# Optimization experiments

Hardware: AMD Instinct MI355X
Metric: run time of the kernel (lower is better)

Reference implementation:

```python
import jax, jax.numpy as jnp
import numpy as np

PAD_IDX = 0
NUM_VISITS, MAX_CODES = 16384, 48
VOCAB, DIM, HID = 20000, 128, 128


def setup_inputs() -> dict:
    key = jax.random.key(0)
    ks = jax.random.split(key, 16)
    ids = jax.random.randint(ks[0], (NUM_VISITS, MAX_CODES), 0, VOCAB)
    # guarantee every visit has at least one non-pad code (original returns
    # zeros for empty visits; we simply avoid that degenerate case)
    ids = ids.at[:, 0].set(jnp.maximum(ids[:, 0], 1))
    s = 0.05
    return {
        "ids": ids,
        "emb": jax.random.normal(ks[1], (VOCAB, DIM), jnp.float32) * s,
        "W1": jax.random.normal(ks[2], (DIM, HID), jnp.float32) * s,
        "b1": jnp.zeros((HID,), jnp.float32),
        "W2": jax.random.normal(ks[3], (HID, HID), jnp.float32) * s,
        "b2": jnp.zeros((HID,), jnp.float32),
        "Wa1": jax.random.normal(ks[4], (HID, HID), jnp.float32) * s,
        "ba1": jnp.zeros((HID,), jnp.float32),
        "wa2": jax.random.normal(ks[5], (HID,), jnp.float32) * s,
        "ba2": jnp.zeros((1,), jnp.float32),
        "Wr1": jax.random.normal(ks[6], (HID, HID), jnp.float32) * s,
        "br1": jnp.zeros((HID,), jnp.float32),
        "Wr2": jax.random.normal(ks[7], (HID, DIM), jnp.float32) * s,
        "br2": jnp.zeros((DIM,), jnp.float32),
    }


def reference(ids, emb, W1, b1, W2, b2, Wa1, ba1, wa2, ba2, Wr1, br1, Wr2, br2):
    # ids: [V, C] padded code indices; pad_idx codes are masked out.
    mask = ids != PAD_IDX                              # [V, C]
    x = emb[ids]                                       # [V, C, D]
    # phi: Linear->SiLU->Linear->SiLU
    h = jax.nn.silu(x @ W1 + b1)
    h = jax.nn.silu(h @ W2 + b2)                       # [V, C, H]
    # attention pooling: Linear->Tanh->Linear(1), masked softmax over codes
    a = jnp.tanh(h @ Wa1 + ba1) @ wa2 + ba2[0]         # [V, C]
    a = jnp.where(mask, a, -jnp.inf)
    a = jax.nn.softmax(a, axis=1)                      # pad rows -> weight 0
    h_pool = jnp.einsum("vc,vch->vh", a, h)            # [V, H]
    # rho: Linear->SiLU->Linear
    v = jax.nn.silu(h_pool @ Wr1 + br1) @ Wr2 + br2    # [V, D]
    return v
```

## Files before the change

kernel.cpp:

```cpp
#include <hip/hip_runtime.h>
#include <math.h>


#define DIM 128
#define MT 16
#define XLDP 136

typedef float f32x4 __attribute__((ext_vector_type(4)));
typedef short short8 __attribute__((ext_vector_type(8)));
typedef unsigned short u16x8 __attribute__((ext_vector_type(8)));

#define MFMA(a, b, c) __builtin_amdgcn_mfma_f32_16x16x32_bf16(a, b, c, 0, 0, 0)

__device__ __forceinline__ float fast_rcp(float x) {
  return __builtin_amdgcn_rcpf(x);
}
__device__ __forceinline__ float silu_f(float v) {
  return v * fast_rcp(1.0f + __expf(-v));
}
__device__ __forceinline__ float tanh_f(float v) {
  float t = __expf(2.0f * v);
  return 1.0f - 2.0f * fast_rcp(t + 1.0f);
}

__device__ __forceinline__ unsigned short bf16_hi(float x, float* hif) {
  unsigned u = __builtin_bit_cast(unsigned, x);
  unsigned h = (u + 0x8000u) >> 16;
  *hif = __builtin_bit_cast(float, h << 16);
  return (unsigned short)h;
}
__device__ __forceinline__ unsigned short bf16_rd(float x) {
  unsigned u = __builtin_bit_cast(unsigned, x);
  return (unsigned short)((u + 0x8000u) >> 16);
}
__device__ __forceinline__ unsigned short f2h(float x) {
  return __builtin_bit_cast(unsigned short, (_Float16)x);
}
__device__ __forceinline__ float h2f(unsigned short u) {
  return (float)__builtin_bit_cast(_Float16, u);
}

__global__ __launch_bounds__(256) void prep_wfrags(
    const float* __restrict__ W1, const float* __restrict__ W2,
    const float* __restrict__ Wa1, const float* __restrict__ Wr1,
    const float* __restrict__ Wr2, unsigned short* __restrict__ frags) {
  const int m = blockIdx.x >> 3, chunk = blockIdx.x & 7;
  const float* W = (m == 0) ? W1 : (m == 1) ? W2 : (m == 2) ? Wa1
                  : (m == 3) ? Wr1 : Wr2;
  unsigned short* fh = frags + (size_t)m * 32768;
  unsigned short* fl = fh + 16384;
  const int fid = chunk * 256 + threadIdx.x;
  const int lane = fid & 63, s = (fid >> 6) & 3, t = fid >> 8;
  const int k0 = s * 32 + (lane >> 4) * 8;
  const int n = t * 16 + (lane & 15);
#pragma unroll
  for (int j = 0; j < 8; ++j) {
    float w = W[(size_t)(k0 + j) * DIM + n];
    float hf;
    unsigned short h = bf16_hi(w, &hf);
    fh[fid * 8 + j] = h;
    fl[fid * 8 + j] = bf16_rd(w - hf);
  }
}

__device__ __forceinline__ void stage_bf16(const float* __restrict__ src,
                                           unsigned short (*xh)[XLDP],
                                           unsigned short (*xl)[XLDP],
                                           int tid) {
  const float4* s = (const float4*)src;
#pragma unroll
  for (int tph = 0; tph < 2; ++tph) {
    int idx = tid + tph * 256;
    int r = idx >> 5, c4 = idx & 31;
    float4 v = s[idx];
    float hf;
    ushort4 h, l;
    h.x = bf16_hi(v.x, &hf); l.x = bf16_rd(v.x - hf);
    h.y = bf16_hi(v.y, &hf); l.y = bf16_rd(v.y - hf);
    h.z = bf16_hi(v.z, &hf); l.z = bf16_rd(v.z - hf);
    h.w = bf16_hi(v.w, &hf); l.w = bf16_rd(v.w - hf);
    *(ushort4*)&xh[r][c4 * 4] = h;
    *(ushort4*)&xl[r][c4 * 4] = l;
  }
}

template <int NT>
__device__ __forceinline__ void gemm_frag(const unsigned short (*xh)[XLDP],
                                          const unsigned short (*xl)[XLDP],
                                          const unsigned short* __restrict__ bhp,
                                          const unsigned short* __restrict__ blp,
                                          int tt0, int lane, f32x4 acc[NT]) {
  const int cr = lane & 15, g = lane >> 4;
  short8 ah[4], al[4];
#pragma unroll
  for (int s = 0; s < 4; ++s) {
    ah[s] = *(const short8*)&xh[cr][s * 32 + g * 8];
    al[s] = *(const short8*)&xl[cr][s * 32 + g * 8];
  }
#pragma unroll
  for (int t = 0; t < NT; ++t) {
    short8 bh[4], bl[4];
#pragma unroll
    for (int s = 0; s < 4; ++s) {
      bh[s] = *(const short8*)(bhp +
          ((size_t)((tt0 + t) * 4 + s) * 64 + lane) * 8);
      bl[s] = *(const short8*)(blp +
          ((size_t)((tt0 + t) * 4 + s) * 64 + lane) * 8);
    }
    f32x4 a0 = {0.f, 0.f, 0.f, 0.f}, a1 = {0.f, 0.f, 0.f, 0.f};
#pragma unroll
    for (int s = 0; s < 4; ++s) {
      a0 = MFMA(ah[s], bh[s], a0);
      a1 = MFMA(ah[s], bl[s], a1);
      a1 = MFMA(al[s], bh[s], a1);
    }
    acc[t] = a0 + a1;
  }
}

__global__ __launch_bounds__(256) void vocab_mfma(
    const float* __restrict__ emb, const unsigned short* __restrict__ frags,
    const float* __restrict__ b1, const float* __restrict__ b2,
    const float* __restrict__ ba1, const float* __restrict__ wa2,
    const float* __restrict__ ba2, unsigned short* __restrict__ H2h,
    float* __restrict__ L) {
  __shared__ unsigned short Xh[2][MT][XLDP], Xl[2][MT][XLDP];
  __shared__ float sP[4][MT];
  const int tid = threadIdx.x, wid = tid >> 6, lane = tid & 63;
  const int cr = lane & 15, g = lane >> 4;
  const int m0 = blockIdx.x * MT;

  stage_bf16(emb + (size_t)m0 * DIM, Xh[0], Xl[0], tid);
  __syncthreads();

  f32x4 acc[2];
  gemm_frag<2>(Xh[0], Xl[0], frags, frags + 16384, wid * 2, lane, acc);
#pragma unroll
  for (int t = 0; t < 2; ++t) {
    const int col = (wid * 2 + t) * 16 + cr;
    const float bv = b1[col];
#pragma unroll
    for (int r = 0; r < 4; ++r) {
      float o = silu_f(acc[t][r] + bv);
      float hf;
      Xh[1][g * 4 + r][col] = bf16_hi(o, &hf);
      Xl[1][g * 4 + r][col] = bf16_rd(o - hf);
    }
  }
  __syncthreads();
  gemm_frag<2>(Xh[1], Xl[1], frags + 32768, frags + 32768 + 16384,
               wid * 2, lane, acc);
#pragma unroll
  for (int t = 0; t < 2; ++t) {
    const int col = (wid * 2 + t) * 16 + cr;
    const float bv = b2[col];
#pragma unroll
    for (int r = 0; r < 4; ++r) {
      float o = silu_f(acc[t][r] + bv);
      float hf;
      const int row = g * 4 + r;
      Xh[0][row][col] = bf16_hi(o, &hf);
      Xl[0][row][col] = bf16_rd(o - hf);
      H2h[(size_t)(m0 + row) * DIM + col] = f2h(o);
    }
  }
  __syncthreads();
  gemm_frag<2>(Xh[0], Xl[0], frags + 65536, frags + 65536 + 16384,
               wid * 2, lane, acc);
  {
    float pl[4] = {0.f, 0.f, 0.f, 0.f};
#pragma unroll
    for (int t = 0; t < 2; ++t) {
      const int col = (wid * 2 + t) * 16 + cr;
      const float bav = ba1[col], wav = wa2[col];
#pragma unroll
      for (int r = 0; r < 4; ++r)
        pl[r] = fmaf(tanh_f(acc[t][r] + bav), wav, pl[r]);
    }
#pragma unroll
    for (int r = 0; r < 4; ++r) {
      float p = pl[r];
      p += __shfl_xor(p, 1, 64);
      p += __shfl_xor(p, 2, 64);
      p += __shfl_xor(p, 4, 64);
      p += __shfl_xor(p, 8, 64);
      if (cr == 0) sP[wid][g * 4 + r] = p;
    }
  }
  __syncthreads();
  if (tid < MT)
    L[m0 + tid] = sP[0][tid] + sP[1][tid] + sP[2][tid] + sP[3][tid] + ba2[0];
}

__global__ __launch_bounds__(512, 4) void pool_rho(
    const int* __restrict__ ids, const float* __restrict__ L,
    const unsigned short* __restrict__ H2h,
    const unsigned short* __restrict__ frags,
    const float* __restrict__ br1, const float* __restrict__ br2,
    float* __restrict__ out) {
  __shared__ unsigned short Xh[2][MT][XLDP], Xl[2][MT][XLDP];
  const int tid = threadIdx.x, wid = tid >> 6, lane = tid & 63;
  const int cr = lane & 15, g = lane >> 4;
  const int li = lane & 15;
  const int m0 = blockIdx.x * MT;

  const int vi0 = wid * 2, vi1 = vi0 + 1;
  const int v0 = m0 + vi0, v1 = m0 + vi1;

  int id0 = 0, id1 = 0;
  float lg0 = -3.4e38f, lg1 = -3.4e38f;
  if (lane < 48) {
    id0 = ids[(size_t)v0 * 48 + lane];
    id1 = ids[(size_t)v1 * 48 + lane];
    if (id0 != 0) lg0 = L[id0];
    if (id1 != 0) lg1 = L[id1];
  }
  float mx0 = lg0, mx1 = lg1;
#pragma unroll
  for (int m = 32; m; m >>= 1) {
    mx0 = fmaxf(mx0, __shfl_xor(mx0, m, 64));
    mx1 = fmaxf(mx1, __shfl_xor(mx1, m, 64));
  }
  float e0 = (lg0 > -3.0e38f) ? __expf(lg0 - mx0) : 0.f;
  float e1 = (lg1 > -3.0e38f) ? __expf(lg1 - mx1) : 0.f;
  float s0 = e0, s1 = e1;
#pragma unroll
  for (int m = 32; m; m >>= 1) {
    s0 += __shfl_xor(s0, m, 64);
    s1 += __shfl_xor(s1, m, 64);
  }
  const float a0 = e0 / s0, a1 = e1 / s1;

  float p0[8] = {0.f, 0.f, 0.f, 0.f, 0.f, 0.f, 0.f, 0.f};
  float p1[8] = {0.f, 0.f, 0.f, 0.f, 0.f, 0.f, 0.f, 0.f};
#pragma unroll 6
  for (int c = 0; c < 12; ++c) {
    const int cc = 4 * c + g;
    const float ac0 = __shfl(a0, cc, 64);
    const int ic0 = __shfl(id0, cc, 64);
    const float ac1 = __shfl(a1, cc, 64);
    const int ic1 = __shfl(id1, cc, 64);
    const u16x8 h0 = *(const u16x8*)(H2h + (size_t)ic0 * DIM + li * 8);
    const u16x8 h1 = *(const u16x8*)(H2h + (size_t)ic1 * DIM + li * 8);
#pragma unroll
    for (int j = 0; j < 8; ++j) {
      p0[j] = fmaf(ac0, h2f(h0[j]), p0[j]);
      p1[j] = fmaf(ac1, h2f(h1[j]), p1[j]);
    }
  }
#pragma unroll
  for (int j = 0; j < 8; ++j) {
    p0[j] += __shfl_xor(p0[j], 16, 64);
    p0[j] += __shfl_xor(p0[j], 32, 64);
    p1[j] += __shfl_xor(p1[j], 16, 64);
    p1[j] += __shfl_xor(p1[j], 32, 64);
  }
  if (lane < 16) {
    u16x8 hh0, hl0, hh1, hl1;
#pragma unroll
    for (int j = 0; j < 8; ++j) {
      float hf;
      hh0[j] = bf16_hi(p0[j], &hf);
      hl0[j] = bf16_rd(p0[j] - hf);
      hh1[j] = bf16_hi(p1[j], &hf);
      hl1[j] = bf16_rd(p1[j] - hf);
    }
    *(u16x8*)&Xh[0][vi0][li * 8] = hh0;
    *(u16x8*)&Xl[0][vi0][li * 8] = hl0;
    *(u16x8*)&Xh[0][vi1][li * 8] = hh1;
    *(u16x8*)&Xl[0][vi1][li * 8] = hl1;
  }
  __syncthreads();

  f32x4 acc2[1];
  gemm_frag<1>(Xh[0], Xl[0], frags + 3 * 32768, frags + 3 * 32768 + 16384,
               wid, lane, acc2);
  {
    const int col = wid * 16 + cr;
    const float bv = br1[col];
#pragma unroll
    for (int r = 0; r < 4; ++r) {
      float o = silu_f(acc2[0][r] + bv);
      float hf;
      Xh[1][g * 4 + r][col] = bf16_hi(o, &hf);
      Xl[1][g * 4 + r][col] = bf16_rd(o - hf);
    }
  }
  __syncthreads();
  gemm_frag<1>(Xh[1], Xl[1], frags + 4 * 32768, frags + 4 * 32768 + 16384,
               wid, lane, acc2);
  {
    const int col = wid * 16 + cr;
    const float bv = br2[col];
#pragma unroll
    for (int r = 0; r < 4; ++r)
      out[(size_t)(m0 + g * 4 + r) * DIM + col] = acc2[0][r] + bv;
  }
}

extern "C" void kernel_launch(void* const* d_in, const int* in_sizes, int n_in,
                              void* d_out, int out_size, void* d_ws,
                              size_t ws_size, hipStream_t stream) {
  const int*   ids = (const int*)  d_in[0];
  const float* emb = (const float*)d_in[1];
  const float* W1  = (const float*)d_in[2];
  const float* b1  = (const float*)d_in[3];
  const float* W2  = (const float*)d_in[4];
  const float* b2  = (const float*)d_in[5];
  const float* Wa1 = (const float*)d_in[6];
  const float* ba1 = (const float*)d_in[7];
  const float* wa2 = (const float*)d_in[8];
  const float* ba2 = (const float*)d_in[9];
  const float* Wr1 = (const float*)d_in[10];
  const float* br1 = (const float*)d_in[11];
  const float* Wr2 = (const float*)d_in[12];
  const float* br2 = (const float*)d_in[13];
  float* out = (float*)d_out;

  const int VOCAB = 20000, V = 16384;

  unsigned short* H2h = (unsigned short*)d_ws;
  float* L = (float*)(H2h + (size_t)VOCAB * DIM);
  unsigned short* frags = (unsigned short*)(L + VOCAB);

  prep_wfrags<<<40, 256, 0, stream>>>(W1, W2, Wa1, Wr1, Wr2, frags);
  vocab_mfma<<<VOCAB / MT, 256, 0, stream>>>(emb, frags, b1, b2, ba1, wa2,
                                             ba2, H2h, L);
  pool_rho<<<V / MT, 512, 0, stream>>>(ids, L, H2h, frags, br1, br2, out);
}
```

Measured before the change: 122.2 us.

## Widen vocab MLP tile to 32 rows with 8 waves reusing B fragments

The per-vocab MLP kernel now processes 32 embedding rows per block with 512 threads. Each wave owns one 16-column output strip and loads its weight fragments once, reusing them across two 16-row strips. This halves the weight-fragment traffic per row and cuts the block count. The cost is more LDS per block and fewer blocks in the grid, and 20000/32 still divides evenly.

```diff
diff --git a/kernel.cpp b/kernel.cpp
--- a/kernel.cpp
+++ b/kernel.cpp
@@ -4,6 +4,7 @@
 
 #define DIM 128
 #define MT 16
+#define MT2 32
 #define XLDP 136
 
 typedef float f32x4 __attribute__((ext_vector_type(4)));
@@ -63,24 +64,124 @@
   }
 }
 
-__device__ __forceinline__ void stage_bf16(const float* __restrict__ src,
-                                           unsigned short (*xh)[XLDP],
-                                           unsigned short (*xl)[XLDP],
-                                           int tid) {
-  const float4* s = (const float4*)src;
-#pragma unroll
-  for (int tph = 0; tph < 2; ++tph) {
-    int idx = tid + tph * 256;
-    int r = idx >> 5, c4 = idx & 31;
-    float4 v = s[idx];
-    float hf;
-    ushort4 h, l;
-    h.x = bf16_hi(v.x, &hf); l.x = bf16_rd(v.x - hf);
-    h.y = bf16_hi(v.y, &hf); l.y = bf16_rd(v.y - hf);
-    h.z = bf16_hi(v.z, &hf); l.z = bf16_rd(v.z - hf);
-    h.w = bf16_hi(v.w, &hf); l.w = bf16_rd(v.w - hf);
-    *(ushort4*)&xh[r][c4 * 4] = h;
-    *(ushort4*)&xl[r][c4 * 4] = l;
+__device__ __forceinline__ void loadB(const unsigned short* __restrict__ bhp,
+                                      const unsigned short* __restrict__ blp,
+                                      int tt, int lane, short8 bh[4],
+                                      short8 bl[4]) {
+#pragma unroll
+  for (int s = 0; s < 4; ++s) {
+    bh[s] = *(const short8*)(bhp + ((size_t)(tt * 4 + s) * 64 + lane) * 8);
+    bl[s] = *(const short8*)(blp + ((size_t)(tt * 4 + s) * 64 + lane) * 8);
+  }
+}
+
+__device__ __forceinline__ f32x4 gemm_strip(const unsigned short (*xh)[XLDP],
+                                            const unsigned short (*xl)[XLDP],
+                                            int st, const short8 bh[4],
+                                            const short8 bl[4], int lane) {
+  const int cr = lane & 15, g = lane >> 4;
+  f32x4 a0 = {0.f, 0.f, 0.f, 0.f}, a1 = {0.f, 0.f, 0.f, 0.f};
+#pragma unroll
+  for (int s = 0; s < 4; ++s) {
+    short8 ah = *(const short8*)&xh[st * 16 + cr][s * 32 + g * 8];
+    short8 al = *(const short8*)&xl[st * 16 + cr][s * 32 + g * 8];
+    a0 = MFMA(ah, bh[s], a0);
+    a1 = MFMA(ah, bl[s], a1);
+    a1 = MFMA(al, bh[s], a1);
+  }
+  return a0 + a1;
+}
+
+__global__ __launch_bounds__(512, 4) void vocab_mfma(
+    const float* __restrict__ emb, const unsigned short* __restrict__ frags,
+    const float* __restrict__ b1, const float* __restrict__ b2,
+    const float* __restrict__ ba1, const float* __restrict__ wa2,
+    const float* __restrict__ ba2, unsigned short* __restrict__ H2h,
+    float* __restrict__ L) {
+  __shared__ unsigned short Xh[2][MT2][XLDP], Xl[2][MT2][XLDP];
+  __shared__ float sP[8][MT2];
+  const int tid = threadIdx.x, wid = tid >> 6, lane = tid & 63;
+  const int cr = lane & 15, g = lane >> 4;
+  const int m0 = blockIdx.x * MT2;
+  const int col = wid * 16 + cr;
+
+  {
+    const float4* s = (const float4*)(emb + (size_t)m0 * DIM);
+#pragma unroll
+    for (int tph = 0; tph < 2; ++tph) {
+      int idx = tid + tph * 512;
+      int r = idx >> 5, c4 = idx & 31;
+      float4 v = s[idx];
+      float hf;
+      ushort4 h, l;
+      h.x = bf16_hi(v.x, &hf); l.x = bf16_rd(v.x - hf);
+      h.y = bf16_hi(v.y, &hf); l.y = bf16_rd(v.y - hf);
+      h.z = bf16_hi(v.z, &hf); l.z = bf16_rd(v.z - hf);
+      h.w = bf16_hi(v.w, &hf); l.w = bf16_rd(v.w - hf);
+      *(ushort4*)&Xh[0][r][c4 * 4] = h;
+      *(ushort4*)&Xl[0][r][c4 * 4] = l;
+    }
+  }
+  __syncthreads();
+
+  short8 bh[4], bl[4];
+  loadB(frags, frags + 16384, wid, lane, bh, bl);
+  {
+    const float bv = b1[col];
+#pragma unroll
+    for (int st = 0; st < 2; ++st) {
+      f32x4 acc = gemm_strip(Xh[0], Xl[0], st, bh, bl, lane);
+#pragma unroll
+      for (int r = 0; r < 4; ++r) {
+        float o = silu_f(acc[r] + bv);
+        float hf;
+        Xh[1][st * 16 + g * 4 + r][col] = bf16_hi(o, &hf);
+        Xl[1][st * 16 + g * 4 + r][col] = bf16_rd(o - hf);
+      }
+    }
+  }
+  __syncthreads();
+  loadB(frags + 32768, frags + 32768 + 16384, wid, lane, bh, bl);
+  {
+    const float bv = b2[col];
+#pragma unroll
+    for (int st = 0; st < 2; ++st) {
+      f32x4 acc = gemm_strip(Xh[1], Xl[1], st, bh, bl, lane);
+#pragma unroll
+      for (int r = 0; r < 4; ++r) {
+        float o = silu_f(acc[r] + bv);
+        float hf;
+        const int row = st * 16 + g * 4 + r;
+        Xh[0][row][col] = bf16_hi(o, &hf);
+        Xl[0][row][col] = bf16_rd(o - hf);
+        H2h[(size_t)(m0 + row) * DIM + col] = f2h(o);
+      }
+    }
+  }
+  __syncthreads();
+  loadB(frags + 65536, frags + 65536 + 16384, wid, lane, bh, bl);
+  {
+    const float bav = ba1[col], wav = wa2[col];
+#pragma unroll
+    for (int st = 0; st < 2; ++st) {
+      f32x4 acc = gemm_strip(Xh[0], Xl[0], st, bh, bl, lane);
+#pragma unroll
+      for (int r = 0; r < 4; ++r) {
+        float p = tanh_f(acc[r] + bav) * wav;
+        p += __shfl_xor(p, 1, 64);
+        p += __shfl_xor(p, 2, 64);
+        p += __shfl_xor(p, 4, 64);
+        p += __shfl_xor(p, 8, 64);
+        if (cr == 0) sP[wid][st * 16 + g * 4 + r] = p;
+      }
+    }
+  }
+  __syncthreads();
+  if (tid < MT2) {
+    float s = ba2[0];
+#pragma unroll
+    for (int w = 0; w < 8; ++w) s += sP[w][tid];
+    L[m0 + tid] = s;
   }
 }
 
@@ -116,80 +217,6 @@
     }
     acc[t] = a0 + a1;
   }
-}
-
-__global__ __launch_bounds__(256) void vocab_mfma(
-    const float* __restrict__ emb, const unsigned short* __restrict__ frags,
-    const float* __restrict__ b1, const float* __restrict__ b2,
-    const float* __restrict__ ba1, const float* __restrict__ wa2,
-    const float* __restrict__ ba2, unsigned short* __restrict__ H2h,
-    float* __restrict__ L) {
-  __shared__ unsigned short Xh[2][MT][XLDP], Xl[2][MT][XLDP];
-  __shared__ float sP[4][MT];
-  const int tid = threadIdx.x, wid = tid >> 6, lane = tid & 63;
-  const int cr = lane & 15, g = lane >> 4;
-  const int m0 = blockIdx.x * MT;
-
-  stage_bf16(emb + (size_t)m0 * DIM, Xh[0], Xl[0], tid);
-  __syncthreads();
-
-  f32x4 acc[2];
-  gemm_frag<2>(Xh[0], Xl[0], frags, frags + 16384, wid * 2, lane, acc);
-#pragma unroll
-  for (int t = 0; t < 2; ++t) {
-    const int col = (wid * 2 + t) * 16 + cr;
-    const float bv = b1[col];
-#pragma unroll
-    for (int r = 0; r < 4; ++r) {
-      float o = silu_f(acc[t][r] + bv);
-      float hf;
-      Xh[1][g * 4 + r][col] = bf16_hi(o, &hf);
-      Xl[1][g * 4 + r][col] = bf16_rd(o - hf);
-    }
-  }
-  __syncthreads();
-  gemm_frag<2>(Xh[1], Xl[1], frags + 32768, frags + 32768 + 16384,
-               wid * 2, lane, acc);
-#pragma unroll
-  for (int t = 0; t < 2; ++t) {
-    const int col = (wid * 2 + t) * 16 + cr;
-    const float bv = b2[col];
-#pragma unroll
-    for (int r = 0; r < 4; ++r) {
-      float o = silu_f(acc[t][r] + bv);
-      float hf;
-      const int row = g * 4 + r;
-      Xh[0][row][col] = bf16_hi(o, &hf);
-      Xl[0][row][col] = bf16_rd(o - hf);
-      H2h[(size_t)(m0 + row) * DIM + col] = f2h(o);
-    }
-  }
-  __syncthreads();
-  gemm_frag<2>(Xh[0], Xl[0], frags + 65536, frags + 65536 + 16384,
-               wid * 2, lane, acc);
-  {
-    float pl[4] = {0.f, 0.f, 0.f, 0.f};
-#pragma unroll
-    for (int t = 0; t < 2; ++t) {
-      const int col = (wid * 2 + t) * 16 + cr;
-      const float bav = ba1[col], wav = wa2[col];
-#pragma unroll
-      for (int r = 0; r < 4; ++r)
-        pl[r] = fmaf(tanh_f(acc[t][r] + bav), wav, pl[r]);
-    }
-#pragma unroll
-    for (int r = 0; r < 4; ++r) {
-      float p = pl[r];
-      p += __shfl_xor(p, 1, 64);
-      p += __shfl_xor(p, 2, 64);
-      p += __shfl_xor(p, 4, 64);
-      p += __shfl_xor(p, 8, 64);
-      if (cr == 0) sP[wid][g * 4 + r] = p;
-    }
-  }
-  __syncthreads();
-  if (tid < MT)
-    L[m0 + tid] = sP[0][tid] + sP[1][tid] + sP[2][tid] + sP[3][tid] + ba2[0];
 }
 
 __global__ __launch_bounds__(512, 4) void pool_rho(
@@ -324,7 +351,7 @@
   unsigned short* frags = (unsigned short*)(L + VOCAB);
 
   prep_wfrags<<<40, 256, 0, stream>>>(W1, W2, Wa1, Wr1, Wr2, frags);
-  vocab_mfma<<<VOCAB / MT, 256, 0, stream>>>(emb, frags, b1, b2, ba1, wa2,
-                                             ba2, H2h, L);
+  vocab_mfma<<<VOCAB / MT2, 512, 0, stream>>>(emb, frags, b1, b2, ba1, wa2,
+                                              ba2, H2h, L);
   pool_rho<<<V / MT, 512, 0, stream>>>(ids, L, H2h, frags, br1, br2, out);
 }
```

Measured after the change: 121.6 us. Within noise of the previous version (-0.5%).
